# Kernel tuning notes

Measured on AMD Instinct MI355X. Metric: run time of the kernel, lower is better.

## Reference

```python
import jax, jax.numpy as jnp
import numpy as np

B, N, D, H, L = 128, 256, 256, 8, 4      # graphs, nodes/graph, hidden, heads, layers
NTOT = B * N                              # 32768 nodes
E = 1048576                               # edges (avg degree 32)
DIN = 64
DH = D // H
BN_EPS = 1e-5
BN_SCALE = 1.0 / np.sqrt(1.0 + BN_EPS)    # eval BN with running mean 0, var 1


def _bn(h, g, b):
    # eval-mode BatchNorm1d: (h - 0)/sqrt(1 + eps) * g + b
    return h * (g * BN_SCALE) + b


def setup_inputs() -> dict:
    key = jax.random.key(0)
    ks = jax.random.split(key, 32)
    s = 0.02
    x = jax.random.normal(ks[0], (NTOT, DIN), jnp.float32)
    # within-graph random edges: dst lives in the same graph as src
    src = jax.random.randint(ks[1], (E,), 0, NTOT, dtype=jnp.int32)
    dst = (src // N) * N + jax.random.randint(ks[2], (E,), 0, N, dtype=jnp.int32)
    edge_index = jnp.stack([src, dst])
    edge_attr = jax.random.uniform(ks[3], (E,), jnp.float32)
    batch = jnp.arange(NTOT, dtype=jnp.int32) // N
    inp = {
        "x": x,
        "edge_attr": edge_attr,
        "node_w": s * jax.random.normal(ks[4], (DIN, D), jnp.float32),
        "node_b": jnp.zeros((D,), jnp.float32),
        "edge_w": s * jax.random.normal(ks[5], (1, D), jnp.float32),
        "edge_b": jnp.zeros((D,), jnp.float32),
        "gine_w1": s * jax.random.normal(ks[6], (L, D, D), jnp.float32),
        "gine_b1": jnp.zeros((L, D), jnp.float32),
        "gine_w2": s * jax.random.normal(ks[7], (L, D, D), jnp.float32),
        "gine_b2": jnp.zeros((L, D), jnp.float32),
        "attn_in_w": s * jax.random.normal(ks[8], (L, D, 3 * D), jnp.float32),
        "attn_in_b": jnp.zeros((L, 3 * D), jnp.float32),
        "attn_out_w": s * jax.random.normal(ks[9], (L, D, D), jnp.float32),
        "attn_out_b": jnp.zeros((L, D), jnp.float32),
        "mlp_w1": s * jax.random.normal(ks[10], (L, D, 2 * D), jnp.float32),
        "mlp_b1": jnp.zeros((L, 2 * D), jnp.float32),
        "mlp_w2": s * jax.random.normal(ks[11], (L, 2 * D, D), jnp.float32),
        "mlp_b2": jnp.zeros((L, D), jnp.float32),
        "bn1_g": 1.0 + 0.1 * jax.random.normal(ks[12], (L, D), jnp.float32),
        "bn1_b": jnp.zeros((L, D), jnp.float32),
        "bn2_g": 1.0 + 0.1 * jax.random.normal(ks[13], (L, D), jnp.float32),
        "bn2_b": jnp.zeros((L, D), jnp.float32),
        "bn3_g": 1.0 + 0.1 * jax.random.normal(ks[14], (L, D), jnp.float32),
        "bn3_b": jnp.zeros((L, D), jnp.float32),
        "edge_index": edge_index,
        "batch": batch,
    }
    return inp


def reference(x, edge_attr, node_w, node_b, edge_w, edge_b,
              gine_w1, gine_b1, gine_w2, gine_b2,
              attn_in_w, attn_in_b, attn_out_w, attn_out_b,
              mlp_w1, mlp_b1, mlp_w2, mlp_b2,
              bn1_g, bn1_b, bn2_g, bn2_b, bn3_g, bn3_b,
              edge_index, batch):
    src, dst = edge_index[0], edge_index[1]
    h = x @ node_w + node_b                                  # [NTOT, D]
    e = edge_attr[:, None] * edge_w[0] + edge_b              # [E, D] (Linear(1, D))
    scale = 1.0 / np.sqrt(DH)
    for l in range(L):
        # --- GINEConv: out = mlp((1+eps)*x + sum_j relu(x_j + e_ij)), eps=0 ---
        msg = jax.nn.relu(h[src] + e)                        # [E, D] gather
        agg = jax.ops.segment_sum(msg, dst, num_segments=NTOT)  # scatter-add
        z = h + agg
        z = jax.nn.relu(z @ gine_w1[l] + gine_b1[l]) @ gine_w2[l] + gine_b2[l]
        h1 = _bn(z + h, bn1_g[l], bn1_b[l])                  # local branch + residual
        # --- global multi-head self-attention per graph (dense batch, no padding) ---
        hd = h.reshape(B, N, D)
        qkv = hd @ attn_in_w[l] + attn_in_b[l]               # [B, N, 3D]
        q, k, v = jnp.split(qkv, 3, axis=-1)
        q = q.reshape(B, N, H, DH).transpose(0, 2, 1, 3)     # [B, H, N, DH]
        k = k.reshape(B, N, H, DH).transpose(0, 2, 1, 3)
        v = v.reshape(B, N, H, DH).transpose(0, 2, 1, 3)
        attn = jax.nn.softmax(jnp.einsum('bhqd,bhkd->bhqk', q, k) * scale, axis=-1)
        o = jnp.einsum('bhqk,bhkd->bhqd', attn, v).transpose(0, 2, 1, 3).reshape(B, N, D)
        o = (o @ attn_out_w[l] + attn_out_b[l]).reshape(NTOT, D)
        h2 = _bn(o + h, bn2_g[l], bn2_b[l])                  # global branch + residual
        # --- combine + FFN ---
        out = h1 + h2
        out = out + (jax.nn.relu(out @ mlp_w1[l] + mlp_b1[l]) @ mlp_w2[l] + mlp_b2[l])
        h = _bn(out, bn3_g[l], bn3_b[l])
    return h
```

## Files before the change

### kernel.cpp

```cpp
#include <hip/hip_runtime.h>
#include <math.h>

#define NTOT   32768
#define DMODEL 256
#define EDGES  1048576
#define BGRAPH 128
#define NNODE  256
#define NHEAD  8
#define DHEAD  32
#define NLAYER 4
#define DIN    64
#define BNS    0.9999950000374997f
#define CAPG   9216

typedef short bf16x8 __attribute__((ext_vector_type(8)));
typedef float f32x4  __attribute__((ext_vector_type(4)));

__device__ __forceinline__ unsigned short f2b(float f) {
    union { float f; unsigned int u; } v; v.f = f;
    unsigned int r = v.u + 0x7FFFu + ((v.u >> 16) & 1u);
    return (unsigned short)(r >> 16);
}
__device__ __forceinline__ float b2f(unsigned short u) {
    union { unsigned int u; float f; } v; v.u = ((unsigned int)u) << 16;
    return v.f;
}

__global__ __launch_bounds__(1024)
void k_bucket(const int* __restrict__ src, const int* __restrict__ dst,
              const float* __restrict__ ea, int* __restrict__ gcnt,
              uint2* __restrict__ gbuf) {
    __shared__ int hist[BGRAPH], base[BGRAPH], cur[BGRAPH];
    int t = threadIdx.x;
    int e0 = blockIdx.x * 4096;
    if (t < BGRAPH) { hist[t] = 0; cur[t] = 0; }
    __syncthreads();
    int g4[4]; unsigned int m4[4], a4[4];
#pragma unroll
    for (int j = 0; j < 4; ++j) {
        int e = e0 + j * 1024 + t;
        int s = src[e], d = dst[e];
        g4[j] = d >> 8;
        m4[j] = (unsigned int)(s & 255) | ((unsigned int)(d & 255) << 16);
        a4[j] = __float_as_uint(ea[e]);
        atomicAdd(&hist[g4[j]], 1);
    }
    __syncthreads();
    if (t < BGRAPH) base[t] = atomicAdd(&gcnt[t], hist[t]);
    __syncthreads();
#pragma unroll
    for (int j = 0; j < 4; ++j) {
        int g = g4[j];
        int slot = base[g] + atomicAdd(&cur[g], 1);
        if (slot < CAPG) {
            uint2 r; r.x = m4[j]; r.y = a4[j];
            gbuf[(size_t)g * CAPG + slot] = r;
        }
    }
}

__global__ __launch_bounds__(1024)
void k_gsort(const uint2* __restrict__ gbuf, const int* __restrict__ gcnt,
             uint2* __restrict__ epk, int* __restrict__ rowptr) {
    __shared__ int s[NNODE], excl[NNODE + 1], cur[NNODE];
    int g = blockIdx.x;
    int c = gcnt[g];
    int t = threadIdx.x;
    size_t base = (size_t)g * CAPG;
    if (t < NNODE) { s[t] = 0; cur[t] = 0; }
    __syncthreads();
    for (int i = t; i < c; i += 1024)
        atomicAdd(&s[gbuf[base + i].x >> 16], 1);
    __syncthreads();
    for (int o = 1; o < NNODE; o <<= 1) {
        int add = (t < NNODE && t >= o) ? s[t - o] : 0;
        __syncthreads();
        if (t < NNODE) s[t] += add;
        __syncthreads();
    }
    if (t < NNODE) excl[t + 1] = s[t];
    if (t == 0) excl[0] = 0;
    __syncthreads();
    if (t <= NNODE) rowptr[g * (NNODE + 1) + t] = (int)base + excl[t];
    for (int i = t; i < c; i += 1024) {
        uint2 r = gbuf[base + i];
        int dl = r.x >> 16;
        int p = excl[dl] + atomicAdd(&cur[dl], 1);
        epk[base + p] = r;
    }
}

__global__ __launch_bounds__(256)
void k_convall(const float* __restrict__ node_w, const float* __restrict__ gine_w1,
               const float* __restrict__ gine_w2, const float* __restrict__ attn_out_w,
               const float* __restrict__ attn_in_w, const float* __restrict__ mlp_w1,
               const float* __restrict__ mlp_w2,
               const float* __restrict__ bn1_g, const float* __restrict__ bn1_b,
               const float* __restrict__ bn2_g, const float* __restrict__ bn2_b,
               const float* __restrict__ bn3_g, const float* __restrict__ bn3_b,
               const float* __restrict__ gb2, const float* __restrict__ aob,
               const float* __restrict__ mb2, const float* __restrict__ x,
               unsigned short* __restrict__ w_node, unsigned short* __restrict__ w_g1,
               unsigned short* __restrict__ w_cat, unsigned short* __restrict__ w_ai,
               unsigned short* __restrict__ w_m1, unsigned short* __restrict__ w_m2s,
               float* __restrict__ biasC, float* __restrict__ rC,
               float* __restrict__ biasF, float* __restrict__ rF,
               unsigned short* __restrict__ xb) {
    __shared__ float tile[32][33];
    int bid = blockIdx.x;
    int t = threadIdx.x;

    if (bid >= 2580) {
        int i = ((bid - 2580) * 256 + t) * 4;
        float4 v = *(const float4*)(x + i);
        xb[i + 0] = f2b(v.x); xb[i + 1] = f2b(v.y);
        xb[i + 2] = f2b(v.z); xb[i + 3] = f2b(v.w);
        return;
    }
    if (bid >= 2576) {
        int i = (bid - 2576) * 256 + t;
        float s1 = bn1_g[i] * BNS, t1 = bn1_b[i];
        float s2 = bn2_g[i] * BNS, t2 = bn2_b[i];
        float s3 = bn3_g[i] * BNS, t3 = bn3_b[i];
        biasC[i] = gb2[i] * s1 + t1 + aob[i] * s2 + t2;
        rC[i]    = s1 + s2;
        biasF[i] = mb2[i] * s3 + t3;
        rF[i]    = s3;
        return;
    }
    const float* src; unsigned short* dst; const float* scale;
    int K_, N_, Kdst, koff, tx, ty, local;
    if (bid < 16)        { local = bid;      src = node_w;     dst = w_node; scale = nullptr; K_ = 64;  N_ = 256; Kdst = 64;  koff = 0;   tx = 8;  ty = 2;  }
    else if (bid < 272)  { local = bid-16;   src = gine_w1;    dst = w_g1;   scale = nullptr; K_ = 256; N_ = 256; Kdst = 256; koff = 0;   tx = 8;  ty = 8;  }
    else if (bid < 528)  { local = bid-272;  src = gine_w2;    dst = w_cat;  scale = bn1_g;   K_ = 256; N_ = 256; Kdst = 512; koff = 0;   tx = 8;  ty = 8;  }
    else if (bid < 784)  { local = bid-528;  src = attn_out_w; dst = w_cat;  scale = bn2_g;   K_ = 256; N_ = 256; Kdst = 512; koff = 256; tx = 8;  ty = 8;  }
    else if (bid < 1552) { local = bid-784;  src = attn_in_w;  dst = w_ai;   scale = nullptr; K_ = 256; N_ = 768; Kdst = 256; koff = 0;   tx = 24; ty = 8;  }
    else if (bid < 2064) { local = bid-1552; src = mlp_w1;     dst = w_m1;   scale = nullptr; K_ = 256; N_ = 512; Kdst = 256; koff = 0;   tx = 16; ty = 8;  }
    else                 { local = bid-2064; src = mlp_w2;     dst = w_m2s;  scale = bn3_g;   K_ = 512; N_ = 256; Kdst = 512; koff = 0;   tx = 8;  ty = 16; }
    int per = tx * ty;
    int l = local / per;
    int rem = local - l * per;
    int kyt = rem / tx, nxt = rem - kyt * tx;
    int n0 = nxt * 32, k0 = kyt * 32;
    const float* s = src + (size_t)l * K_ * N_;
    unsigned short* d = dst + (size_t)l * N_ * Kdst;
    int tx2 = t & 31, ty2 = t >> 5;
#pragma unroll
    for (int i = 0; i < 32; i += 8)
        tile[ty2 + i][tx2] = s[(size_t)(k0 + ty2 + i) * N_ + n0 + tx2];
    __syncthreads();
#pragma unroll
    for (int i = 0; i < 32; i += 8) {
        int n = n0 + ty2 + i;
        float sc = scale ? scale[(size_t)l * N_ + n] * BNS : 1.f;
        d[(size_t)n * Kdst + koff + k0 + tx2] = f2b(tile[tx2][ty2 + i] * sc);
    }
}

__global__ __launch_bounds__(1024)
void k_gine_g1(const unsigned short* __restrict__ hb,
               const int* __restrict__ rowptr, const uint2* __restrict__ epk,
               const float* __restrict__ ew, const float* __restrict__ eb,
               const unsigned short* __restrict__ w1,
               const float* __restrict__ b1,
               unsigned short* __restrict__ hid) {
    __shared__ unsigned short lds_h[NNODE * DMODEL];
    __shared__ uint2 mscr[16][64];
    int g = blockIdx.x >> 1, half = blockIdx.x & 1;
    int t = threadIdx.x;

    const unsigned short* gsrc = hb + (size_t)g * NNODE * DMODEL;
#pragma unroll
    for (int i = 0; i < 8; ++i) {
        int slot = i * 1024 + t;
        __builtin_amdgcn_global_load_lds(
            (const __attribute__((address_space(1))) void*)(gsrc + slot * 8),
            (__attribute__((address_space(3))) void*)&lds_h[slot * 8], 16, 0, 0);
    }
    asm volatile("s_waitcnt vmcnt(0)" ::: "memory");
    __syncthreads();

    int w = t >> 6, lane = t & 63;
    int d0 = lane * 4;
    float4 ew4 = *(const float4*)&ew[d0];
    float4 eb4 = *(const float4*)&eb[d0];
    uint2* ms = mscr[w];

    const int* rp = rowptr + g * (NNODE + 1);
    int ln0 = half * 128 + w * 8;
    unsigned int zlo[8], zhi[8];
#pragma unroll 1
    for (int i = 0; i < 8; ++i) {
        int ln = ln0 + i;
        int beg = rp[ln], end = rp[ln + 1];
        float a0 = 0.f, a1 = 0.f, a2 = 0.f, a3 = 0.f;
        for (int c = beg; c < end; c += 64) {
            int cnt = min(64, end - c);
            if (lane < cnt) ms[lane] = epk[c + lane];
            asm volatile("s_waitcnt lgkmcnt(0)" ::: "memory");
#pragma unroll 4
            for (int ii = 0; ii < cnt; ++ii) {
                uint2 rec = ms[ii];
                int   sl  = (int)(rec.x & 0xffffu);
                float av  = __uint_as_float(rec.y);
                uint2 hv = *(const uint2*)&lds_h[sl * DMODEL + d0];
                float t0 = fmaf(av, ew4.x, eb4.x);
                float t1 = fmaf(av, ew4.y, eb4.y);
                float t2 = fmaf(av, ew4.z, eb4.z);
                float t3 = fmaf(av, ew4.w, eb4.w);
                a0 += fmaxf(__uint_as_float(hv.x << 16) + t0, 0.f);
                a1 += fmaxf(__uint_as_float(hv.x & 0xffff0000u) + t1, 0.f);
                a2 += fmaxf(__uint_as_float(hv.y << 16) + t2, 0.f);
                a3 += fmaxf(__uint_as_float(hv.y & 0xffff0000u) + t3, 0.f);
            }
        }
        uint2 hv = *(const uint2*)&lds_h[ln * DMODEL + d0];
        float z0 = __uint_as_float(hv.x << 16)         + a0;
        float z1 = __uint_as_float(hv.x & 0xffff0000u) + a1;
        float z2 = __uint_as_float(hv.y << 16)         + a2;
        float z3 = __uint_as_float(hv.y & 0xffff0000u) + a3;
        asm("v_cvt_pk_bf16_f32 %0, %1, %2" : "=v"(zlo[i]) : "v"(z0), "v"(z1));
        asm("v_cvt_pk_bf16_f32 %0, %1, %2" : "=v"(zhi[i]) : "v"(z2), "v"(z3));
    }
    __syncthreads();

    char* zs = (char*)lds_h;
#pragma unroll
    for (int i = 0; i < 8; ++i) {
        int r = w * 8 + i;
        int pq = (lane >> 1) ^ (r & 7);
        uint2 pk; pk.x = zlo[i]; pk.y = zhi[i];
        *(uint2*)(zs + r * 512 + (pq << 4) + ((lane & 1) << 3)) = pk;
    }
    __syncthreads();

    int wr2 = w >> 3, wc2 = w & 7;
    int rl = lane & 15, kc = lane >> 4;
    f32x4 acc[4][2] = {};
#pragma unroll
    for (int kq = 0; kq < 8; ++kq) {
        bf16x8 av[4], bv[2];
#pragma unroll
        for (int mm = 0; mm < 4; ++mm) {
            int r = wr2 * 64 + mm * 16 + rl;
            int pq = (kq * 4 + kc) ^ (r & 7);
            av[mm] = *(const bf16x8*)(zs + r * 512 + (pq << 4));
        }
#pragma unroll
        for (int nn = 0; nn < 2; ++nn) {
            int nrow = wc2 * 32 + nn * 16 + rl;
            bv[nn] = *(const bf16x8*)(w1 + (size_t)nrow * 256 + kq * 32 + kc * 8);
        }
        __builtin_amdgcn_s_setprio(1);
#pragma unroll
        for (int mm = 0; mm < 4; ++mm)
#pragma unroll
            for (int nn = 0; nn < 2; ++nn)
                acc[mm][nn] = __builtin_amdgcn_mfma_f32_16x16x32_bf16(av[mm], bv[nn], acc[mm][nn], 0, 0, 0);
        __builtin_amdgcn_s_setprio(0);
    }
    int rh = lane >> 4;
    size_t rowbase = (size_t)g * NNODE + half * 128;
#pragma unroll
    for (int nn = 0; nn < 2; ++nn) {
        int col = wc2 * 32 + nn * 16 + rl;
        float bb = b1[col];
#pragma unroll
        for (int mm = 0; mm < 4; ++mm) {
#pragma unroll
            for (int j = 0; j < 4; ++j) {
                int r = wr2 * 64 + mm * 16 + rh * 4 + j;
                float v = fmaxf(acc[mm][nn][j] + bb, 0.f);
                hid[(rowbase + r) * 512 + col] = f2b(v);
            }
        }
    }
}

template <int MODE>
__global__ __launch_bounds__(256)
void k_mm(const unsigned short* __restrict__ A, const unsigned short* __restrict__ Bt,
          const float* __restrict__ bias, const float* __restrict__ rvec,
          const unsigned short* __restrict__ resb, float* __restrict__ Cf,
          unsigned short* __restrict__ Cb, int M, int N, int K, int ldc, int gx) {
    const int BM = 128, BN = 128, BK = 64;
    __shared__ unsigned short As[BM * BK];
    __shared__ unsigned short Bs[BN * BK];

    int nwg = gridDim.x;
    int bid = blockIdx.x;
    int logical = (bid & 7) * (nwg >> 3) + (bid >> 3);
    int by = logical / gx, bx = logical % gx;

    int t = threadIdx.x;
    int w = t >> 6, l = t & 63;
    int wr = w >> 1, wc = w & 1;
    int bm = by * BM, bn = bx * BN;

    f32x4 acc[4][4] = {};
    int rl = l & 15, kc = l >> 4;

    for (int k0 = 0; k0 < K; k0 += BK) {
#pragma unroll
        for (int i = 0; i < 4; ++i) {
            int slot = i * 256 + t;
            int row = slot >> 3, pc = slot & 7;
            int lc = pc ^ (row & 7);
            const unsigned short* gp = A + (size_t)(bm + row) * K + k0 + lc * 8;
            __builtin_amdgcn_global_load_lds(
                (const __attribute__((address_space(1))) void*)gp,
                (__attribute__((address_space(3))) void*)&As[(i * 256 + w * 64) * 8],
                16, 0, 0);
        }
#pragma unroll
        for (int i = 0; i < 4; ++i) {
            int slot = i * 256 + t;
            int row = slot >> 3, pc = slot & 7;
            int lc = pc ^ (row & 7);
            const unsigned short* gp = Bt + (size_t)(bn + row) * K + k0 + lc * 8;
            __builtin_amdgcn_global_load_lds(
                (const __attribute__((address_space(1))) void*)gp,
                (__attribute__((address_space(3))) void*)&Bs[(i * 256 + w * 64) * 8],
                16, 0, 0);
        }
        asm volatile("s_waitcnt vmcnt(0)" ::: "memory");
        __syncthreads();

#pragma unroll
        for (int kk = 0; kk < 2; ++kk) {
            int lch = kk * 4 + kc;
            bf16x8 av[4], bv[4];
#pragma unroll
            for (int m = 0; m < 4; ++m) {
                int r = wr * 64 + m * 16 + rl;
                av[m] = *(const bf16x8*)&As[r * BK + ((lch ^ (r & 7)) << 3)];
            }
#pragma unroll
            for (int n = 0; n < 4; ++n) {
                int r = wc * 64 + n * 16 + rl;
                bv[n] = *(const bf16x8*)&Bs[r * BK + ((lch ^ (r & 7)) << 3)];
            }
#pragma unroll
            for (int m = 0; m < 4; ++m)
#pragma unroll
                for (int n = 0; n < 4; ++n)
                    acc[m][n] = __builtin_amdgcn_mfma_f32_16x16x32_bf16(av[m], bv[n], acc[m][n], 0, 0, 0);
        }
        __syncthreads();
    }

    int rh = l >> 4;
#pragma unroll
    for (int n = 0; n < 4; ++n) {
        int col = bn + wc * 64 + n * 16 + rl;
        float bv_ = bias[col];
        float rv = 0.f;
        if (MODE == 4) rv = rvec[col];
#pragma unroll
        for (int m = 0; m < 4; ++m) {
#pragma unroll
            for (int j = 0; j < 4; ++j) {
                int row = bm + wr * 64 + m * 16 + rh * 4 + j;
                size_t idx = (size_t)row * ldc + col;
                float v = acc[m][n][j] + bv_;
                if (MODE == 1) v = fmaxf(v, 0.f);
                if (MODE == 4) v += rv * b2f(resb[idx]);
                if (Cf) Cf[idx] = v;
                Cb[idx] = f2b(v);
            }
        }
    }
}

#define VP 264
#define OSTR 512
#define OOFF 256
__global__ __launch_bounds__(256, 3)
void k_attn(const unsigned short* __restrict__ qkv, unsigned short* __restrict__ o) {
    __shared__ unsigned short lds[8448 + 16896];
    unsigned short* Vt = lds;
    unsigned short* Ps = lds + 8448;

    int bh = blockIdx.x;
    int b = bh >> 3, h = bh & 7;
    int t = threadIdx.x;
    int w = t >> 6, l = t & 63;
    int rl = l & 15, kc = l >> 4;
    const float scale = 0.17677669529663687f;

    const unsigned short* base = qkv + (size_t)b * NNODE * (3 * DMODEL);
    const unsigned short* Kbase = base + DMODEL + h * DHEAD;

    {
        int k0 = (t & 63) * 4, d0 = (t >> 6) * 8;
        bf16x8 vr[4];
#pragma unroll
        for (int i = 0; i < 4; ++i)
            vr[i] = *(const bf16x8*)(base + (size_t)(k0 + i) * (3 * DMODEL) + 2 * DMODEL + h * DHEAD + d0);
#pragma unroll
        for (int d = 0; d < 8; ++d) {
            ushort4 pk;
            pk.x = (unsigned short)vr[0][d];
            pk.y = (unsigned short)vr[1][d];
            pk.z = (unsigned short)vr[2][d];
            pk.w = (unsigned short)vr[3][d];
            *(ushort4*)&Vt[(d0 + d) * VP + k0] = pk;
        }
    }

    bf16x8 qv[4];
#pragma unroll
    for (int m = 0; m < 4; ++m) {
        int q = w * 64 + m * 16 + rl;
        qv[m] = *(const bf16x8*)(base + (size_t)q * (3 * DMODEL) + h * DHEAD + kc * 8);
    }
    __syncthreads();

    unsigned short* Pw = Ps + w * 16 * VP;
    f32x4 zero = {0.f, 0.f, 0.f, 0.f};

#pragma unroll 1
    for (int m = 0; m < 4; ++m) {
        f32x4 s[16];
#pragma unroll
        for (int g4 = 0; g4 < 4; ++g4) {
            bf16x8 kv[4];
#pragma unroll
            for (int i = 0; i < 4; ++i)
                kv[i] = *(const bf16x8*)(Kbase + (size_t)((g4 * 4 + i) * 16 + rl) * (3 * DMODEL) + kc * 8);
            __builtin_amdgcn_s_setprio(1);
#pragma unroll
            for (int i = 0; i < 4; ++i)
                s[g4 * 4 + i] = __builtin_amdgcn_mfma_f32_16x16x32_bf16(kv[i], qv[m], zero, 0, 0, 0);
            __builtin_amdgcn_s_setprio(0);
        }
        float mv = -1e30f;
#pragma unroll
        for (int n = 0; n < 16; ++n)
#pragma unroll
            for (int j = 0; j < 4; ++j) mv = fmaxf(mv, s[n][j]);
        mv = fmaxf(mv, __shfl_xor(mv, 16));
        mv = fmaxf(mv, __shfl_xor(mv, 32));
        float nb = -mv * scale;
        float sumv = 0.f;
#pragma unroll
        for (int n = 0; n < 16; ++n) {
            float p0 = __expf(fmaf(s[n][0], scale, nb));
            float p1 = __expf(fmaf(s[n][1], scale, nb));
            float p2 = __expf(fmaf(s[n][2], scale, nb));
            float p3 = __expf(fmaf(s[n][3], scale, nb));
            sumv += (p0 + p1) + (p2 + p3);
            unsigned int lo, hi;
            asm("v_cvt_pk_bf16_f32 %0, %1, %2" : "=v"(lo) : "v"(p0), "v"(p1));
            asm("v_cvt_pk_bf16_f32 %0, %1, %2" : "=v"(hi) : "v"(p2), "v"(p3));
            uint2 pk; pk.x = lo; pk.y = hi;
            *(uint2*)&Pw[rl * VP + n * 16 + kc * 4] = pk;
        }
        sumv += __shfl_xor(sumv, 16);
        sumv += __shfl_xor(sumv, 32);

        f32x4 o0 = zero, o1 = zero;
#pragma unroll
        for (int ks = 0; ks < 8; ++ks) {
            bf16x8 pa = *(const bf16x8*)&Pw[rl * VP + ks * 32 + kc * 8];
            bf16x8 v0 = *(const bf16x8*)&Vt[rl * VP + ks * 32 + kc * 8];
            bf16x8 v1 = *(const bf16x8*)&Vt[(16 + rl) * VP + ks * 32 + kc * 8];
            __builtin_amdgcn_s_setprio(1);
            o0 = __builtin_amdgcn_mfma_f32_16x16x32_bf16(pa, v0, o0, 0, 0, 0);
            o1 = __builtin_amdgcn_mfma_f32_16x16x32_bf16(pa, v1, o1, 0, 0, 0);
            __builtin_amdgcn_s_setprio(0);
        }
#pragma unroll
        for (int j = 0; j < 4; ++j) {
            float sj = __shfl(sumv, kc * 4 + j);
            float inv = 1.f / sj;
            int q = w * 64 + m * 16 + kc * 4 + j;
            unsigned short* orow = o + ((size_t)b * NNODE + q) * OSTR + OOFF + h * DHEAD;
            orow[rl]      = f2b(o0[j] * inv);
            orow[16 + rl] = f2b(o1[j] * inv);
        }
    }
}

extern "C" void kernel_launch(void* const* d_in, const int* in_sizes, int n_in,
                              void* d_out, int out_size, void* d_ws, size_t ws_size,
                              hipStream_t stream) {
    const float* x          = (const float*)d_in[0];
    const float* edge_attr  = (const float*)d_in[1];
    const float* node_w     = (const float*)d_in[2];
    const float* node_b     = (const float*)d_in[3];
    const float* edge_w     = (const float*)d_in[4];
    const float* edge_b     = (const float*)d_in[5];
    const float* gine_w1    = (const float*)d_in[6];
    const float* gine_b1    = (const float*)d_in[7];
    const float* gine_w2    = (const float*)d_in[8];
    const float* gine_b2    = (const float*)d_in[9];
    const float* attn_in_w  = (const float*)d_in[10];
    const float* attn_in_b  = (const float*)d_in[11];
    const float* attn_out_w = (const float*)d_in[12];
    const float* attn_out_b = (const float*)d_in[13];
    const float* mlp_w1     = (const float*)d_in[14];
    const float* mlp_b1     = (const float*)d_in[15];
    const float* mlp_w2     = (const float*)d_in[16];
    const float* mlp_b2     = (const float*)d_in[17];
    const float* bn1_g      = (const float*)d_in[18];
    const float* bn1_b      = (const float*)d_in[19];
    const float* bn2_g      = (const float*)d_in[20];
    const float* bn2_b      = (const float*)d_in[21];
    const float* bn3_g      = (const float*)d_in[22];
    const float* bn3_b      = (const float*)d_in[23];
    const int*   edge_index = (const int*)d_in[24];

    const int* srcp = edge_index;
    const int* dstp = edge_index + EDGES;

    float* out = (float*)d_out;
    char*  ws  = (char*)d_ws;

    size_t off = 0;
    unsigned short* hb    = (unsigned short*)(ws + off); off += (size_t)NTOT * DMODEL * 2;
    unsigned short* comb2 = (unsigned short*)(ws + off); off += (size_t)NTOT * 512 * 2;
    unsigned short* qkvb  = (unsigned short*)(ws + off); off += (size_t)NTOT * 768 * 2;
    unsigned short* cmbb  = (unsigned short*)(ws + off); off += (size_t)NTOT * DMODEL * 2;
    unsigned short* h5b   = (unsigned short*)(ws + off); off += (size_t)NTOT * 512 * 2;
    unsigned short* xb    = (unsigned short*)(ws + off); off += (size_t)NTOT * DIN * 2;
    unsigned short* w_node = (unsigned short*)(ws + off); off += (size_t)DMODEL * DIN * 2;
    unsigned short* w_g1   = (unsigned short*)(ws + off); off += (size_t)NLAYER * DMODEL * DMODEL * 2;
    unsigned short* w_cat  = (unsigned short*)(ws + off); off += (size_t)NLAYER * DMODEL * 512 * 2;
    unsigned short* w_ai   = (unsigned short*)(ws + off); off += (size_t)NLAYER * 3 * DMODEL * DMODEL * 2;
    unsigned short* w_m1   = (unsigned short*)(ws + off); off += (size_t)NLAYER * 2 * DMODEL * DMODEL * 2;
    unsigned short* w_m2s  = (unsigned short*)(ws + off); off += (size_t)NLAYER * DMODEL * 512 * 2;
    float* biasC = (float*)(ws + off); off += (size_t)NLAYER * DMODEL * 4;
    float* rC    = (float*)(ws + off); off += (size_t)NLAYER * DMODEL * 4;
    float* biasF = (float*)(ws + off); off += (size_t)NLAYER * DMODEL * 4;
    float* rF    = (float*)(ws + off); off += (size_t)NLAYER * DMODEL * 4;
    uint2* gbuf  = (uint2*)(ws + off);  off += (size_t)BGRAPH * CAPG * 8;
    uint2* epk   = (uint2*)(ws + off);  off += (size_t)BGRAPH * CAPG * 8;
    int*   gcnt  = (int*)(ws + off);    off += (size_t)BGRAPH * 4;
    int*   rowptr = (int*)(ws + off);   off += (size_t)BGRAPH * (NNODE + 1) * 4;
    (void)ws_size; (void)in_sizes; (void)n_in; (void)out_size;

    hipMemsetAsync(gcnt, 0, (size_t)BGRAPH * 4, stream);
    k_bucket<<<EDGES / 4096, 1024, 0, stream>>>(srcp, dstp, edge_attr, gcnt, gbuf);
    k_gsort<<<BGRAPH, 1024, 0, stream>>>(gbuf, gcnt, epk, rowptr);

    k_convall<<<4628, 256, 0, stream>>>(node_w, gine_w1, gine_w2, attn_out_w,
                                        attn_in_w, mlp_w1, mlp_w2,
                                        bn1_g, bn1_b, bn2_g, bn2_b, bn3_g, bn3_b,
                                        gine_b2, attn_out_b, mlp_b2, x,
                                        w_node, w_g1, w_cat, w_ai, w_m1, w_m2s,
                                        biasC, rC, biasF, rF, xb);

    k_mm<0><<<2 * (NTOT / 128), 256, 0, stream>>>(
        xb, w_node, node_b, nullptr, nullptr, nullptr, hb, NTOT, DMODEL, DIN, DMODEL, 2);

    for (int l = 0; l < NLAYER; ++l) {
        const unsigned short* g1 = w_g1 + (size_t)l * DMODEL * DMODEL;
        const unsigned short* wc = w_cat + (size_t)l * DMODEL * 512;
        const unsigned short* ai = w_ai + (size_t)l * 3 * DMODEL * DMODEL;
        const unsigned short* m1 = w_m1 + (size_t)l * 2 * DMODEL * DMODEL;
        const unsigned short* m2 = w_m2s + (size_t)l * DMODEL * 512;

        k_gine_g1<<<BGRAPH * 2, 1024, 0, stream>>>(hb, rowptr, epk, edge_w, edge_b,
                                                   g1, gine_b1 + (size_t)l * DMODEL, comb2);
        k_mm<0><<<6 * (NTOT / 128), 256, 0, stream>>>(
            hb, ai, attn_in_b + (size_t)l * 3 * DMODEL, nullptr, nullptr, nullptr,
            qkvb, NTOT, 3 * DMODEL, DMODEL, 3 * DMODEL, 6);
        k_attn<<<BGRAPH * NHEAD, 256, 0, stream>>>(qkvb, comb2);
        k_mm<4><<<2 * (NTOT / 128), 256, 0, stream>>>(
            comb2, wc, biasC + (size_t)l * DMODEL, rC + (size_t)l * DMODEL, hb,
            nullptr, cmbb, NTOT, DMODEL, 512, DMODEL, 2);
        k_mm<1><<<4 * (NTOT / 128), 256, 0, stream>>>(
            cmbb, m1, mlp_b1 + (size_t)l * 2 * DMODEL, nullptr, nullptr, nullptr,
            h5b, NTOT, 2 * DMODEL, DMODEL, 2 * DMODEL, 4);
        float* dest = (l == NLAYER - 1) ? out : nullptr;
        k_mm<4><<<2 * (NTOT / 128), 256, 0, stream>>>(
            h5b, m2, biasF + (size_t)l * DMODEL, rF + (size_t)l * DMODEL, cmbb,
            dest, hb, NTOT, DMODEL, 512, DMODEL, 2);
    }
}
```

Measured before the change: 836.7 us.

## Fuse QKV projection into attention kernel and prefetch edge records in GINE

Removes the separate QKV GEMM launch and its global qkv buffer. Each (graph, head) block now computes its own Q, K and V slices from the hidden states with MFMA and keeps K and V^T in LDS, which also removes the strided global K loads. The block index is remapped so blocks sharing a head are spread across XCDs. In the GINE aggregation, rowptr values are loaded once and the next chunk of edge records is software-prefetched one chunk ahead. In exchange, each block rereads the graph's hidden rows from global memory for every head. It also uses more LDS, so fewer blocks fit per CU (launch bounds drop to 2).

```diff
diff --git a/kernel.cpp b/kernel.cpp
--- a/kernel.cpp
+++ b/kernel.cpp
@@ -188,15 +188,35 @@
 
     const int* rp = rowptr + g * (NNODE + 1);
     int ln0 = half * 128 + w * 8;
+    int begs[9];
+#pragma unroll
+    for (int i = 0; i < 9; ++i) begs[i] = rp[ln0 + i];
+
+    int ppi = 0, ppc = begs[0];
+    uint2 pf; pf.x = 0; pf.y = 0;
+    {
+        while (ppi < 8 && ppc >= begs[ppi + 1]) { ++ppi; if (ppi < 8) ppc = begs[ppi]; }
+        if (ppi < 8) {
+            int cc = min(64, begs[ppi + 1] - ppc);
+            if (lane < cc) pf = epk[ppc + lane];
+            ppc += 64;
+        }
+    }
+
     unsigned int zlo[8], zhi[8];
 #pragma unroll 1
     for (int i = 0; i < 8; ++i) {
-        int ln = ln0 + i;
-        int beg = rp[ln], end = rp[ln + 1];
+        int beg = begs[i], end = begs[i + 1];
         float a0 = 0.f, a1 = 0.f, a2 = 0.f, a3 = 0.f;
         for (int c = beg; c < end; c += 64) {
             int cnt = min(64, end - c);
-            if (lane < cnt) ms[lane] = epk[c + lane];
+            if (lane < cnt) ms[lane] = pf;
+            while (ppi < 8 && ppc >= begs[ppi + 1]) { ++ppi; if (ppi < 8) ppc = begs[ppi]; }
+            if (ppi < 8) {
+                int cc = min(64, begs[ppi + 1] - ppc);
+                if (lane < cc) pf = epk[ppc + lane];
+                ppc += 64;
+            }
             asm volatile("s_waitcnt lgkmcnt(0)" ::: "memory");
 #pragma unroll 4
             for (int ii = 0; ii < cnt; ++ii) {
@@ -214,11 +234,13 @@
                 a3 += fmaxf(__uint_as_float(hv.y & 0xffff0000u) + t3, 0.f);
             }
         }
-        uint2 hv = *(const uint2*)&lds_h[ln * DMODEL + d0];
-        float z0 = __uint_as_float(hv.x << 16)         + a0;
-        float z1 = __uint_as_float(hv.x & 0xffff0000u) + a1;
-        float z2 = __uint_as_float(hv.y << 16)         + a2;
-        float z3 = __uint_as_float(hv.y & 0xffff0000u) + a3;
+        uint2 hv = *(const uint2*)&lds_h[(ln0 - half * 128 + half * 128 + i) * DMODEL + d0];
+        (void)hv;
+        uint2 hv2 = *(const uint2*)&lds_h[(ln0 + i) * DMODEL + d0];
+        float z0 = __uint_as_float(hv2.x << 16)         + a0;
+        float z1 = __uint_as_float(hv2.x & 0xffff0000u) + a1;
+        float z2 = __uint_as_float(hv2.y << 16)         + a2;
+        float z3 = __uint_as_float(hv2.y & 0xffff0000u) + a3;
         asm("v_cvt_pk_bf16_f32 %0, %1, %2" : "=v"(zlo[i]) : "v"(z0), "v"(z1));
         asm("v_cvt_pk_bf16_f32 %0, %1, %2" : "=v"(zhi[i]) : "v"(z2), "v"(z3));
     }
@@ -372,68 +394,117 @@
     }
 }
 
+#define KP 40
 #define VP 264
 #define OSTR 512
 #define OOFF 256
-__global__ __launch_bounds__(256, 3)
-void k_attn(const unsigned short* __restrict__ qkv, unsigned short* __restrict__ o) {
-    __shared__ unsigned short lds[8448 + 16896];
-    unsigned short* Vt = lds;
-    unsigned short* Ps = lds + 8448;
-
-    int bh = blockIdx.x;
-    int b = bh >> 3, h = bh & 7;
+__global__ __launch_bounds__(256, 2)
+void k_qkv_attn(const unsigned short* __restrict__ hb,
+                const unsigned short* __restrict__ wai,
+                const float* __restrict__ aib,
+                unsigned short* __restrict__ o) {
+    __shared__ unsigned short Ks[256 * KP];
+    __shared__ unsigned short Vt[32 * VP];
+    __shared__ unsigned short Ps[4 * 16 * VP];
+    int bid = blockIdx.x;
+    int logical = (bid & 7) * (BGRAPH * NHEAD / 8) + (bid >> 3);
+    int g = logical >> 3, h = logical & 7;
     int t = threadIdx.x;
     int w = t >> 6, l = t & 63;
-    int rl = l & 15, kc = l >> 4;
+    int rl = l & 15, kc = l >> 4, rh = l >> 4;
     const float scale = 0.17677669529663687f;
-
-    const unsigned short* base = qkv + (size_t)b * NNODE * (3 * DMODEL);
-    const unsigned short* Kbase = base + DMODEL + h * DHEAD;
+    const unsigned short* hg = hb + (size_t)g * NNODE * DMODEL;
+    f32x4 zero = {0.f, 0.f, 0.f, 0.f};
 
     {
-        int k0 = (t & 63) * 4, d0 = (t >> 6) * 8;
-        bf16x8 vr[4];
-#pragma unroll
-        for (int i = 0; i < 4; ++i)
-            vr[i] = *(const bf16x8*)(base + (size_t)(k0 + i) * (3 * DMODEL) + 2 * DMODEL + h * DHEAD + d0);
-#pragma unroll
-        for (int d = 0; d < 8; ++d) {
-            ushort4 pk;
-            pk.x = (unsigned short)vr[0][d];
-            pk.y = (unsigned short)vr[1][d];
-            pk.z = (unsigned short)vr[2][d];
-            pk.w = (unsigned short)vr[3][d];
-            *(ushort4*)&Vt[(d0 + d) * VP + k0] = pk;
-        }
-    }
-
+        f32x4 kacc[4][2] = {};
+        f32x4 vacc[2][4] = {};
+        for (int ks_ = 0; ks_ < 8; ++ks_) {
+            bf16x8 hr[4], wk[2], wv[2];
+#pragma unroll
+            for (int mm = 0; mm < 4; ++mm)
+                hr[mm] = *(const bf16x8*)&hg[(size_t)(w * 64 + mm * 16 + rl) * DMODEL + ks_ * 32 + kc * 8];
+#pragma unroll
+            for (int nn = 0; nn < 2; ++nn) {
+                wk[nn] = *(const bf16x8*)&wai[(size_t)(256 + h * 32 + nn * 16 + rl) * DMODEL + ks_ * 32 + kc * 8];
+                wv[nn] = *(const bf16x8*)&wai[(size_t)(512 + h * 32 + nn * 16 + rl) * DMODEL + ks_ * 32 + kc * 8];
+            }
+            __builtin_amdgcn_s_setprio(1);
+#pragma unroll
+            for (int mm = 0; mm < 4; ++mm)
+#pragma unroll
+                for (int nn = 0; nn < 2; ++nn) {
+                    kacc[mm][nn] = __builtin_amdgcn_mfma_f32_16x16x32_bf16(hr[mm], wk[nn], kacc[mm][nn], 0, 0, 0);
+                    vacc[nn][mm] = __builtin_amdgcn_mfma_f32_16x16x32_bf16(wv[nn], hr[mm], vacc[nn][mm], 0, 0, 0);
+                }
+            __builtin_amdgcn_s_setprio(0);
+        }
+#pragma unroll
+        for (int nn = 0; nn < 2; ++nn) {
+            float bk = aib[256 + h * 32 + nn * 16 + rl];
+#pragma unroll
+            for (int mm = 0; mm < 4; ++mm)
+#pragma unroll
+                for (int j = 0; j < 4; ++j)
+                    Ks[(w * 64 + mm * 16 + rh * 4 + j) * KP + nn * 16 + rl] = f2b(kacc[mm][nn][j] + bk);
+        }
+#pragma unroll
+        for (int nn = 0; nn < 2; ++nn)
+#pragma unroll
+            for (int mm = 0; mm < 4; ++mm)
+#pragma unroll
+                for (int j = 0; j < 4; ++j) {
+                    int dim = nn * 16 + rh * 4 + j;
+                    Vt[dim * VP + w * 64 + mm * 16 + rl] = f2b(vacc[nn][mm][j] + aib[512 + h * 32 + dim]);
+                }
+    }
+
+    unsigned short* Pw = Ps + w * 16 * VP;
+    unsigned short* Qs = Pw;
+    {
+        f32x4 qacc[4][2] = {};
+        for (int ks_ = 0; ks_ < 8; ++ks_) {
+            bf16x8 hr[4], wq[2];
+#pragma unroll
+            for (int mm = 0; mm < 4; ++mm)
+                hr[mm] = *(const bf16x8*)&hg[(size_t)(w * 64 + mm * 16 + rl) * DMODEL + ks_ * 32 + kc * 8];
+#pragma unroll
+            for (int nn = 0; nn < 2; ++nn)
+                wq[nn] = *(const bf16x8*)&wai[(size_t)(h * 32 + nn * 16 + rl) * DMODEL + ks_ * 32 + kc * 8];
+            __builtin_amdgcn_s_setprio(1);
+#pragma unroll
+            for (int mm = 0; mm < 4; ++mm)
+#pragma unroll
+                for (int nn = 0; nn < 2; ++nn)
+                    qacc[mm][nn] = __builtin_amdgcn_mfma_f32_16x16x32_bf16(hr[mm], wq[nn], qacc[mm][nn], 0, 0, 0);
+            __builtin_amdgcn_s_setprio(0);
+        }
+#pragma unroll
+        for (int nn = 0; nn < 2; ++nn) {
+            float bq = aib[h * 32 + nn * 16 + rl];
+#pragma unroll
+            for (int mm = 0; mm < 4; ++mm)
+#pragma unroll
+                for (int j = 0; j < 4; ++j)
+                    Qs[(mm * 16 + rh * 4 + j) * 32 + nn * 16 + rl] = f2b(qacc[mm][nn][j] + bq);
+        }
+    }
     bf16x8 qv[4];
 #pragma unroll
-    for (int m = 0; m < 4; ++m) {
-        int q = w * 64 + m * 16 + rl;
-        qv[m] = *(const bf16x8*)(base + (size_t)q * (3 * DMODEL) + h * DHEAD + kc * 8);
-    }
-    __syncthreads();
-
-    unsigned short* Pw = Ps + w * 16 * VP;
-    f32x4 zero = {0.f, 0.f, 0.f, 0.f};
+    for (int m = 0; m < 4; ++m)
+        qv[m] = *(const bf16x8*)&Qs[(m * 16 + rl) * 32 + kc * 8];
+    __syncthreads();
 
 #pragma unroll 1
     for (int m = 0; m < 4; ++m) {
         f32x4 s[16];
-#pragma unroll
-        for (int g4 = 0; g4 < 4; ++g4) {
-            bf16x8 kv[4];
-#pragma unroll
-            for (int i = 0; i < 4; ++i)
-                kv[i] = *(const bf16x8*)(Kbase + (size_t)((g4 * 4 + i) * 16 + rl) * (3 * DMODEL) + kc * 8);
-            __builtin_amdgcn_s_setprio(1);
-#pragma unroll
-            for (int i = 0; i < 4; ++i)
-                s[g4 * 4 + i] = __builtin_amdgcn_mfma_f32_16x16x32_bf16(kv[i], qv[m], zero, 0, 0, 0);
-            __builtin_amdgcn_s_setprio(0);
-        }
+        __builtin_amdgcn_s_setprio(1);
+#pragma unroll
+        for (int n = 0; n < 16; ++n) {
+            bf16x8 kv = *(const bf16x8*)&Ks[(n * 16 + rl) * KP + kc * 8];
+            s[n] = __builtin_amdgcn_mfma_f32_16x16x32_bf16(kv, qv[m], zero, 0, 0, 0);
+        }
+        __builtin_amdgcn_s_setprio(0);
         float mv = -1e30f;
 #pragma unroll
         for (int n = 0; n < 16; ++n)
@@ -475,7 +546,7 @@
             float sj = __shfl(sumv, kc * 4 + j);
             float inv = 1.f / sj;
             int q = w * 64 + m * 16 + kc * 4 + j;
-            unsigned short* orow = o + ((size_t)b * NNODE + q) * OSTR + OOFF + h * DHEAD;
+            unsigned short* orow = o + ((size_t)g * NNODE + q) * OSTR + OOFF + h * DHEAD;
             orow[rl]      = f2b(o0[j] * inv);
             orow[16 + rl] = f2b(o1[j] * inv);
         }
@@ -520,7 +591,6 @@
     size_t off = 0;
     unsigned short* hb    = (unsigned short*)(ws + off); off += (size_t)NTOT * DMODEL * 2;
     unsigned short* comb2 = (unsigned short*)(ws + off); off += (size_t)NTOT * 512 * 2;
-    unsigned short* qkvb  = (unsigned short*)(ws + off); off += (size_t)NTOT * 768 * 2;
     unsigned short* cmbb  = (unsigned short*)(ws + off); off += (size_t)NTOT * DMODEL * 2;
     unsigned short* h5b   = (unsigned short*)(ws + off); off += (size_t)NTOT * 512 * 2;
     unsigned short* xb    = (unsigned short*)(ws + off); off += (size_t)NTOT * DIN * 2;
@@ -563,10 +633,8 @@
 
         k_gine_g1<<<BGRAPH * 2, 1024, 0, stream>>>(hb, rowptr, epk, edge_w, edge_b,
                                                    g1, gine_b1 + (size_t)l * DMODEL, comb2);
-        k_mm<0><<<6 * (NTOT / 128), 256, 0, stream>>>(
-            hb, ai, attn_in_b + (size_t)l * 3 * DMODEL, nullptr, nullptr, nullptr,
-            qkvb, NTOT, 3 * DMODEL, DMODEL, 3 * DMODEL, 6);
-        k_attn<<<BGRAPH * NHEAD, 256, 0, stream>>>(qkvb, comb2);
+        k_qkv_attn<<<BGRAPH * NHEAD, 256, 0, stream>>>(
+            hb, ai, attn_in_b + (size_t)l * 3 * DMODEL, comb2);
         k_mm<4><<<2 * (NTOT / 128), 256, 0, stream>>>(
             comb2, wc, biasC + (size_t)l * DMODEL, rC + (size_t)l * DMODEL, hb,
             nullptr, cmbb, NTOT, DMODEL, 512, DMODEL, 2);
```

Result: slower. 901.6 us (+7.7%).

## Fuse combine GEMM and FFN GEMMs into one per-row-tile tail kernel

Applied to the files above, without the earlier changes.

Replaces the three GEMM launches after attention (combine projection with residual, FFN up with ReLU, FFN down with residual) with a single kernel. Each 512-thread block owns 128 rows and keeps the combined activations and hidden activations in LDS, streaming weight tiles from global memory. This removes the global round trips for the cmbb and h5b intermediates and two launches. In exchange it uses about 144KB of LDS, which limits occupancy to one block per CU, launches only 256 blocks, and synchronizes on every k-step without double buffering. hb is read for the residual and then overwritten in place, which is safe because each block reads only its own rows before writing them.

```diff
diff --git a/kernel.cpp b/kernel.cpp
--- a/kernel.cpp
+++ b/kernel.cpp
@@ -280,8 +280,7 @@
 template <int MODE>
 __global__ __launch_bounds__(256)
 void k_mm(const unsigned short* __restrict__ A, const unsigned short* __restrict__ Bt,
-          const float* __restrict__ bias, const float* __restrict__ rvec,
-          const unsigned short* __restrict__ resb, float* __restrict__ Cf,
+          const float* __restrict__ bias, float* __restrict__ Cf,
           unsigned short* __restrict__ Cb, int M, int N, int K, int ldc, int gx) {
     const int BM = 128, BN = 128, BK = 64;
     __shared__ unsigned short As[BM * BK];
@@ -354,8 +353,6 @@
     for (int n = 0; n < 4; ++n) {
         int col = bn + wc * 64 + n * 16 + rl;
         float bv_ = bias[col];
-        float rv = 0.f;
-        if (MODE == 4) rv = rvec[col];
 #pragma unroll
         for (int m = 0; m < 4; ++m) {
 #pragma unroll
@@ -364,7 +361,6 @@
                 size_t idx = (size_t)row * ldc + col;
                 float v = acc[m][n][j] + bv_;
                 if (MODE == 1) v = fmaxf(v, 0.f);
-                if (MODE == 4) v += rv * b2f(resb[idx]);
                 if (Cf) Cf[idx] = v;
                 Cb[idx] = f2b(v);
             }
@@ -478,6 +474,176 @@
             unsigned short* orow = o + ((size_t)b * NNODE + q) * OSTR + OOFF + h * DHEAD;
             orow[rl]      = f2b(o0[j] * inv);
             orow[16 + rl] = f2b(o1[j] * inv);
+        }
+    }
+}
+
+template <int LAST>
+__global__ __launch_bounds__(512)
+void k_tail(const unsigned short* __restrict__ comb2,
+            const unsigned short* __restrict__ hbin,
+            const unsigned short* __restrict__ wc,
+            const unsigned short* __restrict__ m1,
+            const unsigned short* __restrict__ m2s,
+            const float* __restrict__ biasC, const float* __restrict__ rC,
+            const float* __restrict__ b1,
+            const float* __restrict__ biasF, const float* __restrict__ rF,
+            unsigned short* __restrict__ hbout, float* __restrict__ outf) {
+    __shared__ unsigned short WS[8192];
+    __shared__ unsigned short cmbS[32768];
+    __shared__ unsigned short hidS[32768];
+    unsigned short* AS = hidS;
+
+    int bm = blockIdx.x * 128;
+    int t = threadIdx.x;
+    int w = t >> 6, l = t & 63;
+    int rl = l & 15, kc = l >> 4;
+    int node = w * 16 + rl;
+    size_t gnode = (size_t)(bm + node);
+    char* cS = (char*)cmbS;
+    char* hS = (char*)hidS;
+
+    f32x4 accC[16] = {};
+
+    {
+        f32x4 accA[16] = {};
+        for (int ks = 0; ks < 16; ++ks) {
+#pragma unroll
+            for (int i = 0; i < 2; ++i) {
+                int slot = i * 512 + t;
+                int row = slot >> 2, q = slot & 3;
+                const unsigned short* gp = wc + (size_t)row * 512 + ks * 32 + ((q ^ (row & 3)) << 3);
+                __builtin_amdgcn_global_load_lds(
+                    (const __attribute__((address_space(1))) void*)gp,
+                    (__attribute__((address_space(3))) void*)&WS[slot * 8], 16, 0, 0);
+            }
+            {
+                int row = t >> 2, q = t & 3;
+                const unsigned short* gp = comb2 + (size_t)(bm + row) * 512 + ks * 32 + ((q ^ (row & 3)) << 3);
+                __builtin_amdgcn_global_load_lds(
+                    (const __attribute__((address_space(1))) void*)gp,
+                    (__attribute__((address_space(3))) void*)&AS[t * 8], 16, 0, 0);
+            }
+            asm volatile("s_waitcnt vmcnt(0)" ::: "memory");
+            __syncthreads();
+            bf16x8 b = *(const bf16x8*)&AS[node * 32 + ((kc ^ (node & 3)) << 3)];
+            __builtin_amdgcn_s_setprio(1);
+#pragma unroll
+            for (int mf = 0; mf < 16; ++mf) {
+                int row = mf * 16 + rl;
+                bf16x8 a = *(const bf16x8*)&WS[row * 32 + ((kc ^ (row & 3)) << 3)];
+                accA[mf] = __builtin_amdgcn_mfma_f32_16x16x32_bf16(a, b, accA[mf], 0, 0, 0);
+            }
+            __builtin_amdgcn_s_setprio(0);
+            __syncthreads();
+        }
+#pragma unroll
+        for (int mf = 0; mf < 16; ++mf) {
+            int dim0 = mf * 16 + kc * 4;
+            float4 bc = *(const float4*)&biasC[dim0];
+            float4 rc = *(const float4*)&rC[dim0];
+            uint2 hv = *(const uint2*)&hbin[gnode * 256 + dim0];
+            float v0 = accA[mf][0] + bc.x + rc.x * __uint_as_float(hv.x << 16);
+            float v1 = accA[mf][1] + bc.y + rc.y * __uint_as_float(hv.x & 0xffff0000u);
+            float v2 = accA[mf][2] + bc.z + rc.z * __uint_as_float(hv.y << 16);
+            float v3 = accA[mf][3] + bc.w + rc.w * __uint_as_float(hv.y & 0xffff0000u);
+            unsigned int lo, hi;
+            asm("v_cvt_pk_bf16_f32 %0, %1, %2" : "=v"(lo) : "v"(v0), "v"(v1));
+            asm("v_cvt_pk_bf16_f32 %0, %1, %2" : "=v"(hi) : "v"(v2), "v"(v3));
+            uint2 pk; pk.x = lo; pk.y = hi;
+            int q = dim0 >> 3, half = (dim0 >> 2) & 1;
+            *(uint2*)(cS + node * 512 + ((q ^ (node & 7)) << 4) + (half << 3)) = pk;
+        }
+    }
+    __syncthreads();
+
+    for (int nh = 0; nh < 2; ++nh) {
+        f32x4 accB[16] = {};
+        for (int ks = 0; ks < 8; ++ks) {
+#pragma unroll
+            for (int i = 0; i < 2; ++i) {
+                int slot = i * 512 + t;
+                int row = slot >> 2, q = slot & 3;
+                const unsigned short* gp = m1 + (size_t)(nh * 256 + row) * 256 + ks * 32 + ((q ^ (row & 3)) << 3);
+                __builtin_amdgcn_global_load_lds(
+                    (const __attribute__((address_space(1))) void*)gp,
+                    (__attribute__((address_space(3))) void*)&WS[slot * 8], 16, 0, 0);
+            }
+            asm volatile("s_waitcnt vmcnt(0)" ::: "memory");
+            __syncthreads();
+            int kq = ks * 4 + kc;
+            bf16x8 b = *(const bf16x8*)(cS + node * 512 + ((kq ^ (node & 7)) << 4));
+            __builtin_amdgcn_s_setprio(1);
+#pragma unroll
+            for (int mf = 0; mf < 16; ++mf) {
+                int row = mf * 16 + rl;
+                bf16x8 a = *(const bf16x8*)&WS[row * 32 + ((kc ^ (row & 3)) << 3)];
+                accB[mf] = __builtin_amdgcn_mfma_f32_16x16x32_bf16(a, b, accB[mf], 0, 0, 0);
+            }
+            __builtin_amdgcn_s_setprio(0);
+            __syncthreads();
+        }
+#pragma unroll
+        for (int mf = 0; mf < 16; ++mf) {
+            int dim0 = mf * 16 + kc * 4;
+            float4 bb = *(const float4*)&b1[nh * 256 + dim0];
+            float v0 = fmaxf(accB[mf][0] + bb.x, 0.f);
+            float v1 = fmaxf(accB[mf][1] + bb.y, 0.f);
+            float v2 = fmaxf(accB[mf][2] + bb.z, 0.f);
+            float v3 = fmaxf(accB[mf][3] + bb.w, 0.f);
+            unsigned int lo, hi;
+            asm("v_cvt_pk_bf16_f32 %0, %1, %2" : "=v"(lo) : "v"(v0), "v"(v1));
+            asm("v_cvt_pk_bf16_f32 %0, %1, %2" : "=v"(hi) : "v"(v2), "v"(v3));
+            uint2 pk; pk.x = lo; pk.y = hi;
+            int q = dim0 >> 3, half = (dim0 >> 2) & 1;
+            *(uint2*)(hS + node * 512 + ((q ^ (node & 7)) << 4) + (half << 3)) = pk;
+        }
+        __syncthreads();
+        for (int ks = 0; ks < 8; ++ks) {
+#pragma unroll
+            for (int i = 0; i < 2; ++i) {
+                int slot = i * 512 + t;
+                int row = slot >> 2, q = slot & 3;
+                const unsigned short* gp = m2s + (size_t)row * 512 + nh * 256 + ks * 32 + ((q ^ (row & 3)) << 3);
+                __builtin_amdgcn_global_load_lds(
+                    (const __attribute__((address_space(1))) void*)gp,
+                    (__attribute__((address_space(3))) void*)&WS[slot * 8], 16, 0, 0);
+            }
+            asm volatile("s_waitcnt vmcnt(0)" ::: "memory");
+            __syncthreads();
+            int kq = ks * 4 + kc;
+            bf16x8 b = *(const bf16x8*)(hS + node * 512 + ((kq ^ (node & 7)) << 4));
+            __builtin_amdgcn_s_setprio(1);
+#pragma unroll
+            for (int mf = 0; mf < 16; ++mf) {
+                int row = mf * 16 + rl;
+                bf16x8 a = *(const bf16x8*)&WS[row * 32 + ((kc ^ (row & 3)) << 3)];
+                accC[mf] = __builtin_amdgcn_mfma_f32_16x16x32_bf16(a, b, accC[mf], 0, 0, 0);
+            }
+            __builtin_amdgcn_s_setprio(0);
+            __syncthreads();
+        }
+    }
+
+#pragma unroll
+    for (int mf = 0; mf < 16; ++mf) {
+        int dim0 = mf * 16 + kc * 4;
+        float4 bf_ = *(const float4*)&biasF[dim0];
+        float4 rf = *(const float4*)&rF[dim0];
+        int q = dim0 >> 3, half = (dim0 >> 2) & 1;
+        uint2 cv = *(const uint2*)(cS + node * 512 + ((q ^ (node & 7)) << 4) + (half << 3));
+        float v0 = accC[mf][0] + bf_.x + rf.x * __uint_as_float(cv.x << 16);
+        float v1 = accC[mf][1] + bf_.y + rf.y * __uint_as_float(cv.x & 0xffff0000u);
+        float v2 = accC[mf][2] + bf_.z + rf.z * __uint_as_float(cv.y << 16);
+        float v3 = accC[mf][3] + bf_.w + rf.w * __uint_as_float(cv.y & 0xffff0000u);
+        unsigned int lo, hi;
+        asm("v_cvt_pk_bf16_f32 %0, %1, %2" : "=v"(lo) : "v"(v0), "v"(v1));
+        asm("v_cvt_pk_bf16_f32 %0, %1, %2" : "=v"(hi) : "v"(v2), "v"(v3));
+        uint2 pk; pk.x = lo; pk.y = hi;
+        *(uint2*)&hbout[gnode * 256 + dim0] = pk;
+        if (LAST) {
+            float4 o4; o4.x = v0; o4.y = v1; o4.z = v2; o4.w = v3;
+            *(float4*)&outf[gnode * 256 + dim0] = o4;
         }
     }
 }
@@ -521,8 +687,6 @@
     unsigned short* hb    = (unsigned short*)(ws + off); off += (size_t)NTOT * DMODEL * 2;
     unsigned short* comb2 = (unsigned short*)(ws + off); off += (size_t)NTOT * 512 * 2;
     unsigned short* qkvb  = (unsigned short*)(ws + off); off += (size_t)NTOT * 768 * 2;
-    unsigned short* cmbb  = (unsigned short*)(ws + off); off += (size_t)NTOT * DMODEL * 2;
-    unsigned short* h5b   = (unsigned short*)(ws + off); off += (size_t)NTOT * 512 * 2;
     unsigned short* xb    = (unsigned short*)(ws + off); off += (size_t)NTOT * DIN * 2;
     unsigned short* w_node = (unsigned short*)(ws + off); off += (size_t)DMODEL * DIN * 2;
     unsigned short* w_g1   = (unsigned short*)(ws + off); off += (size_t)NLAYER * DMODEL * DMODEL * 2;
@@ -552,7 +716,7 @@
                                         biasC, rC, biasF, rF, xb);
 
     k_mm<0><<<2 * (NTOT / 128), 256, 0, stream>>>(
-        xb, w_node, node_b, nullptr, nullptr, nullptr, hb, NTOT, DMODEL, DIN, DMODEL, 2);
+        xb, w_node, node_b, nullptr, hb, NTOT, DMODEL, DIN, DMODEL, 2);
 
     for (int l = 0; l < NLAYER; ++l) {
         const unsigned short* g1 = w_g1 + (size_t)l * DMODEL * DMODEL;
@@ -564,18 +728,22 @@
         k_gine_g1<<<BGRAPH * 2, 1024, 0, stream>>>(hb, rowptr, epk, edge_w, edge_b,
                                                    g1, gine_b1 + (size_t)l * DMODEL, comb2);
         k_mm<0><<<6 * (NTOT / 128), 256, 0, stream>>>(
-            hb, ai, attn_in_b + (size_t)l * 3 * DMODEL, nullptr, nullptr, nullptr,
+            hb, ai, attn_in_b + (size_t)l * 3 * DMODEL, nullptr,
             qkvb, NTOT, 3 * DMODEL, DMODEL, 3 * DMODEL, 6);
         k_attn<<<BGRAPH * NHEAD, 256, 0, stream>>>(qkvb, comb2);
-        k_mm<4><<<2 * (NTOT / 128), 256, 0, stream>>>(
-            comb2, wc, biasC + (size_t)l * DMODEL, rC + (size_t)l * DMODEL, hb,
-            nullptr, cmbb, NTOT, DMODEL, 512, DMODEL, 2);
-        k_mm<1><<<4 * (NTOT / 128), 256, 0, stream>>>(
-            cmbb, m1, mlp_b1 + (size_t)l * 2 * DMODEL, nullptr, nullptr, nullptr,
-            h5b, NTOT, 2 * DMODEL, DMODEL, 2 * DMODEL, 4);
-        float* dest = (l == NLAYER - 1) ? out : nullptr;
-        k_mm<4><<<2 * (NTOT / 128), 256, 0, stream>>>(
-            h5b, m2, biasF + (size_t)l * DMODEL, rF + (size_t)l * DMODEL, cmbb,
-            dest, hb, NTOT, DMODEL, 512, DMODEL, 2);
-    }
-}
+        if (l == NLAYER - 1)
+            k_tail<1><<<NTOT / 128, 512, 0, stream>>>(
+                comb2, hb, wc, m1, m2,
+                biasC + (size_t)l * DMODEL, rC + (size_t)l * DMODEL,
+                mlp_b1 + (size_t)l * 2 * DMODEL,
+                biasF + (size_t)l * DMODEL, rF + (size_t)l * DMODEL,
+                hb, out);
+        else
+            k_tail<0><<<NTOT / 128, 512, 0, stream>>>(
+                comb2, hb, wc, m1, m2,
+                biasC + (size_t)l * DMODEL, rC + (size_t)l * DMODEL,
+                mlp_b1 + (size_t)l * 2 * DMODEL,
+                biasF + (size_t)l * DMODEL, rF + (size_t)l * DMODEL,
+                hb, nullptr);
+    }
+}
```

Result: faster. 793.4 us (-5.2%).
